# Kernel optimization log

Hardware: AMD Instinct MI355X
Metric: run time of the kernel (lower is better)

## Reference

```python
import jax, jax.numpy as jnp
import numpy as np

LEVEL = 3
NUM_BANDS = LEVEL + 1
B, N, D_MODEL, PATCH_NUMS, PRED_LEN = 32, 7, 768, 64, 336

# db4 lowpass decomposition filter (pywt convention)
_DB4_DEC_LO = np.array([
    -0.010597401784997278, 0.032883011666982945, 0.030841381835986965,
    -0.18703481171888114, -0.02798376941698385, 0.6308807679295904,
    0.7148465705525415, 0.23037781330885523], dtype=np.float32)
REC_LO = _DB4_DEC_LO[::-1].copy()                                   # reconstruction lowpass
REC_HI = (_DB4_DEC_LO * ((-1.0) ** (np.arange(8) + 1))).astype(np.float32)  # reconstruction highpass (QMF)


def _upsample2(x):
    # zero-interleave along last axis: (..., L) -> (..., 2L)
    z = jnp.zeros_like(x)
    return jnp.stack([x, z], axis=-1).reshape(*x.shape[:-1], 2 * x.shape[-1])


def _idwt_per(ca, cd, rec_lo, rec_hi):
    # single-level inverse DWT, periodization mode, along last axis: (..., L) -> (..., 2L)
    F = rec_lo.shape[0]
    ua, ud = _upsample2(ca), _upsample2(cd)
    y = jnp.zeros_like(ua)
    for k in range(F):  # small fixed tap loop (F=8)
        y = y + jnp.roll(ua, k, axis=-1) * rec_lo[k] + jnp.roll(ud, k, axis=-1) * rec_hi[k]
    return jnp.roll(y, -(F // 2 - 1), axis=-1)  # compensate filter delay


def _iswt(coeffs, level, rec_lo, rec_hi):
    # coeffs: (..., T, level+1) with bands ordered [cA, cD_level, ..., cD1]
    T = coeffs.shape[-2]
    out = coeffs[..., 0]
    for j in range(level, 0, -1):
        step = 2 ** (j - 1)
        cd = coeffs[..., level - j + 1]
        M = T // step
        # gather the `step` interleaved subsequences as a batch axis: (..., step, M)
        o = jnp.moveaxis(out.reshape(*out.shape[:-1], M, step), -1, -2)
        d = jnp.moveaxis(cd.reshape(*cd.shape[:-1], M, step), -1, -2)
        x1 = _idwt_per(o[..., 0::2], d[..., 0::2], rec_lo, rec_hi)
        x2 = jnp.roll(_idwt_per(o[..., 1::2], d[..., 1::2], rec_lo, rec_hi), 1, axis=-1)
        new = 0.5 * (x1 + x2)  # (..., step, M)
        out = jnp.moveaxis(new, -2, -1).reshape(*out.shape[:-1], T)
    return out


def setup_inputs() -> dict:
    key = jax.random.key(0)
    kx, kw, kb = jax.random.split(key, 3)
    Din = D_MODEL * PATCH_NUMS
    x = jax.random.normal(kx, (B, N, D_MODEL, PATCH_NUMS), dtype=jnp.float32)
    # Linear init ~ U(-1/sqrt(Din), 1/sqrt(Din)); small normal is equivalent for a reference
    W = jax.random.normal(kw, (NUM_BANDS, Din, PRED_LEN), dtype=jnp.float32) * (1.0 / np.sqrt(Din))
    b = jax.random.normal(kb, (NUM_BANDS, PRED_LEN), dtype=jnp.float32) * 0.01
    return {"x": x, "W": W, "b": b}


def reference(x, W, b):
    # x: (B, N, d_model, patch_nums); W: (bands, d_model*patch_nums, pred_len); b: (bands, pred_len)
    Bb, Nn, dm, P = x.shape
    xf = x.reshape(Bb, Nn, dm * P)  # Flatten(start_dim=-2)
    # all band projections as one batched GEMM -> (B, N, pred_len, bands)
    coeffs = jnp.einsum('bnd,kdp->bnpk', xf, W) + b.T
    rec_lo = jnp.asarray(REC_LO)
    rec_hi = jnp.asarray(REC_HI)
    return _iswt(coeffs, LEVEL, rec_lo, rec_hi)  # (B, N, pred_len)
```

## Files before the change

kernel.cpp:

```cpp
#include <hip/hip_runtime.h>
#include <stdint.h>

#define M_ROWS   224
#define K_DIM    49152
#define NCOL     1344
#define PRED     336
#define S_CHUNKS 24
#define STEPS    64


typedef __attribute__((ext_vector_type(8))) short short8;
typedef __attribute__((ext_vector_type(4))) float floatx4;

__device__ __forceinline__ uint16_t f32_to_bf16(float f) {
    uint32_t u = __builtin_bit_cast(uint32_t, f);
    uint32_t r = (u + 0x7fffu + ((u >> 16) & 1u)) >> 16;
    return (uint16_t)r;
}
__device__ __forceinline__ float bf16_to_f32(uint16_t h) {
    uint32_t u = ((uint32_t)h) << 16;
    return __builtin_bit_cast(float, u);
}
__device__ __forceinline__ uint32_t pack2(float lo, float hi) {
    return (uint32_t)f32_to_bf16(lo) | ((uint32_t)f32_to_bf16(hi) << 16);
}

__global__ __launch_bounds__(256, 2) void gemm_partial(
    const float* __restrict__ X,
    const float* __restrict__ W,
    uint16_t* __restrict__ P)
{
    __shared__ uint16_t lA[2][14 * 512];

    const int id = blockIdx.x;
    const int g  = id & 7;
    const int q  = id >> 3;
    const int ct = q % 21;
    const int s  = g + 8 * (q / 21);

    const int tid  = threadIdx.x;
    const int lane = tid & 63;
    const int w    = tid >> 6;
    const int l15  = lane & 15;
    const int kq   = lane >> 4;
    const int c0w  = ct * 64 + w * 16;
    const int band = c0w / PRED;
    const int p0   = c0w - band * PRED;

    const float* wbase = W + (size_t)band * ((size_t)K_DIM * PRED)
                           + (size_t)(kq * 8) * PRED
                           + (size_t)(p0 + l15);
    const float* xbase = X + (size_t)l15 * K_DIM + (size_t)(kq * 8);
    const int kbase = s * (STEPS * 32);

    floatx4 acc[14];
    #pragma unroll
    for (int f = 0; f < 14; ++f) acc[f] = (floatx4){0.f, 0.f, 0.f, 0.f};

    float wcur[8], wnxt[8];
    float4 xr[4][2];

    #pragma unroll
    for (int t = 0; t < 4; ++t) {
        const int f = w + 4 * t;
        if (f < 14) {
            const float* gp = xbase + (size_t)(16 * f) * K_DIM + kbase;
            xr[t][0] = *(const float4*)gp;
            xr[t][1] = *(const float4*)(gp + 4);
        }
    }
    #pragma unroll
    for (int j = 0; j < 8; ++j) wcur[j] = wbase[(size_t)(kbase + j) * PRED];
    #pragma unroll
    for (int t = 0; t < 4; ++t) {
        const int f = w + 4 * t;
        if (f < 14) {
            short8 v;
            ((uint32_t*)&v)[0] = pack2(xr[t][0].x, xr[t][0].y);
            ((uint32_t*)&v)[1] = pack2(xr[t][0].z, xr[t][0].w);
            ((uint32_t*)&v)[2] = pack2(xr[t][1].x, xr[t][1].y);
            ((uint32_t*)&v)[3] = pack2(xr[t][1].z, xr[t][1].w);
            *(short8*)&lA[0][f * 512 + lane * 8] = v;
        }
    }

    for (int st = 0; st < STEPS; ++st) {
        __syncthreads();
        const int cur = st & 1;

        if (st + 1 < STEPS) {
            const int kn = kbase + (st + 1) * 32;
            #pragma unroll
            for (int t = 0; t < 4; ++t) {
                const int f = w + 4 * t;
                if (f < 14) {
                    const float* gp = xbase + (size_t)(16 * f) * K_DIM + kn;
                    xr[t][0] = *(const float4*)gp;
                    xr[t][1] = *(const float4*)(gp + 4);
                }
            }
            #pragma unroll
            for (int j = 0; j < 8; ++j) wnxt[j] = wbase[(size_t)(kn + j) * PRED];
        }

        short8 bfrag;
        #pragma unroll
        for (int j = 0; j < 4; ++j)
            ((uint32_t*)&bfrag)[j] = pack2(wcur[2 * j], wcur[2 * j + 1]);

        #pragma unroll
        for (int f = 0; f < 14; ++f) {
            short8 afrag = *(const short8*)&lA[cur][f * 512 + lane * 8];
            acc[f] = __builtin_amdgcn_mfma_f32_16x16x32_bf16(afrag, bfrag, acc[f], 0, 0, 0);
        }

        if (st + 1 < STEPS) {
            #pragma unroll
            for (int t = 0; t < 4; ++t) {
                const int f = w + 4 * t;
                if (f < 14) {
                    short8 v;
                    ((uint32_t*)&v)[0] = pack2(xr[t][0].x, xr[t][0].y);
                    ((uint32_t*)&v)[1] = pack2(xr[t][0].z, xr[t][0].w);
                    ((uint32_t*)&v)[2] = pack2(xr[t][1].x, xr[t][1].y);
                    ((uint32_t*)&v)[3] = pack2(xr[t][1].z, xr[t][1].w);
                    *(short8*)&lA[cur ^ 1][f * 512 + lane * 8] = v;
                }
            }
            #pragma unroll
            for (int j = 0; j < 8; ++j) wcur[j] = wnxt[j];
        }
    }

    const int col = c0w + l15;
    #pragma unroll
    for (int f = 0; f < 14; ++f) {
        #pragma unroll
        for (int r = 0; r < 4; ++r) {
            const int m = 16 * f + kq * 4 + r;
            P[((size_t)m * S_CHUNKS + s) * NCOL + col] = f32_to_bf16(acc[f][r]);
        }
    }
}

__device__ const float REC_LO[8] = {
     0.23037781330885523f,  0.7148465705525415f,   0.6308807679295904f,
    -0.02798376941698385f, -0.18703481171888114f,  0.030841381835986965f,
     0.032883011666982945f, -0.010597401784997278f };
__device__ const float REC_HI[8] = {
     0.010597401784997278f, 0.032883011666982945f, -0.030841381835986965f,
    -0.18703481171888114f,  0.02798376941698385f,   0.6308807679295904f,
    -0.7148465705525415f,   0.23037781330885523f };

__global__ __launch_bounds__(1024) void reduce_iswt(
    const uint16_t* __restrict__ P,
    const float* __restrict__ bias,
    float* __restrict__ out)
{
    __shared__ float coeff[NCOL];
    __shared__ float buf[2][PRED];

    const int row = blockIdx.x;
    const int tid = threadIdx.x;
    const uint32_t* pr = (const uint32_t*)(P + (size_t)row * S_CHUNKS * NCOL);

    if (tid < NCOL / 2) {
        float a0 = 0.f, a1 = 0.f;
        #pragma unroll 8
        for (int s = 0; s < S_CHUNKS; ++s) {
            const uint32_t v = pr[s * (NCOL / 2) + tid];
            a0 += bf16_to_f32((uint16_t)(v & 0xffff));
            a1 += bf16_to_f32((uint16_t)(v >> 16));
        }
        coeff[2 * tid]     = a0 + bias[2 * tid];
        coeff[2 * tid + 1] = a1 + bias[2 * tid + 1];
    }
    __syncthreads();

    if (tid < PRED) buf[0][tid] = coeff[tid];
    __syncthreads();

    int curb = 0;
    for (int j = 3; j >= 1; --j) {
        const int step = 1 << (j - 1);
        const int M    = PRED / step;
        const float* cd  = &coeff[(4 - j) * PRED];
        const float* cur = buf[curb];
        float* nxt       = buf[curb ^ 1];
        if (tid < PRED) {
            const int t = tid;
            const int sidx = t & (step - 1);
            const int m = t / step;
            const int mm1 = (m == 0) ? (M - 1) : (m - 1);
            float x1 = 0.f, x2 = 0.f;
            #pragma unroll
            for (int k = 0; k < 8; ++k) {
                int i1 = m + 3 - k;  if (i1 < 0) i1 += M; else if (i1 >= M) i1 -= M;
                if ((i1 & 1) == 0) {
                    const int pos = i1 * step + sidx;
                    x1 += cur[pos] * REC_LO[k] + cd[pos] * REC_HI[k];
                }
                int i2 = mm1 + 3 - k;  if (i2 < 0) i2 += M; else if (i2 >= M) i2 -= M;
                if ((i2 & 1) == 0) {
                    const int pos = (i2 + 1) * step + sidx;
                    x2 += cur[pos] * REC_LO[k] + cd[pos] * REC_HI[k];
                }
            }
            nxt[t] = 0.5f * (x1 + x2);
        }
        __syncthreads();
        curb ^= 1;
    }

    if (tid < PRED) out[(size_t)row * PRED + tid] = buf[curb][tid];
}

extern "C" void kernel_launch(void* const* d_in, const int* in_sizes, int n_in,
                              void* d_out, int out_size, void* d_ws, size_t ws_size,
                              hipStream_t stream) {
    const float* X    = (const float*)d_in[0];
    const float* W    = (const float*)d_in[1];
    const float* bias = (const float*)d_in[2];
    float* out        = (float*)d_out;
    uint16_t* P       = (uint16_t*)d_ws;

    gemm_partial<<<21 * S_CHUNKS, 256, 0, stream>>>(X, W, P);
    reduce_iswt <<<M_ROWS, 1024, 0, stream>>>(P, bias, out);
}
```

Before: 518.0 us.

## Double split-K chunks, prefetch W two steps ahead, replace syncthreads with raw barrier

Doubles the number of K chunks, halving the steps per block, and raises the occupancy hint to 4 blocks per CU so more blocks fill the GPU. The main loop is unrolled by two with ping-pong W registers, so W loads are issued two steps ahead. __syncthreads is replaced by an explicit lgkmcnt wait plus s_barrier, which only waits on LDS traffic. The cost is twice as much bf16 partial output to write and reduce, plus tighter register pressure under the new launch bound.

```diff
diff --git a/kernel.cpp b/kernel.cpp
--- a/kernel.cpp
+++ b/kernel.cpp
@@ -5,8 +5,8 @@
 #define K_DIM    49152
 #define NCOL     1344
 #define PRED     336
-#define S_CHUNKS 24
-#define STEPS    64
+#define S_CHUNKS 48
+#define STEPS    32
 
 
 typedef __attribute__((ext_vector_type(8))) short short8;
@@ -22,10 +22,11 @@
     return __builtin_bit_cast(float, u);
 }
 __device__ __forceinline__ uint32_t pack2(float lo, float hi) {
-    return (uint32_t)f32_to_bf16(lo) | ((uint32_t)f32_to_bf16(hi) << 16);
-}
-
-__global__ __launch_bounds__(256, 2) void gemm_partial(
+    uint32_t r = (uint32_t)f32_to_bf16(lo) | ((uint32_t)f32_to_bf16(hi) << 16);
+    return r;
+}
+
+__global__ __launch_bounds__(256, 4) void gemm_partial(
     const float* __restrict__ X,
     const float* __restrict__ W,
     uint16_t* __restrict__ P)
@@ -57,7 +58,7 @@
     #pragma unroll
     for (int f = 0; f < 14; ++f) acc[f] = (floatx4){0.f, 0.f, 0.f, 0.f};
 
-    float wcur[8], wnxt[8];
+    float wA[8], wB[8];
     float4 xr[4][2];
 
     #pragma unroll
@@ -70,7 +71,9 @@
         }
     }
     #pragma unroll
-    for (int j = 0; j < 8; ++j) wcur[j] = wbase[(size_t)(kbase + j) * PRED];
+    for (int j = 0; j < 8; ++j) wA[j] = wbase[(size_t)(kbase + j) * PRED];
+    #pragma unroll
+    for (int j = 0; j < 8; ++j) wB[j] = wbase[(size_t)(kbase + 32 + j) * PRED];
     #pragma unroll
     for (int t = 0; t < 4; ++t) {
         const int f = w + 4 * t;
@@ -83,54 +86,62 @@
             *(short8*)&lA[0][f * 512 + lane * 8] = v;
         }
     }
-
-    for (int st = 0; st < STEPS; ++st) {
-        __syncthreads();
-        const int cur = st & 1;
-
-        if (st + 1 < STEPS) {
-            const int kn = kbase + (st + 1) * 32;
-            #pragma unroll
-            for (int t = 0; t < 4; ++t) {
-                const int f = w + 4 * t;
-                if (f < 14) {
-                    const float* gp = xbase + (size_t)(16 * f) * K_DIM + kn;
-                    xr[t][0] = *(const float4*)gp;
-                    xr[t][1] = *(const float4*)(gp + 4);
-                }
-            }
-            #pragma unroll
-            for (int j = 0; j < 8; ++j) wnxt[j] = wbase[(size_t)(kn + j) * PRED];
-        }
-
-        short8 bfrag;
-        #pragma unroll
-        for (int j = 0; j < 4; ++j)
-            ((uint32_t*)&bfrag)[j] = pack2(wcur[2 * j], wcur[2 * j + 1]);
-
-        #pragma unroll
-        for (int f = 0; f < 14; ++f) {
-            short8 afrag = *(const short8*)&lA[cur][f * 512 + lane * 8];
-            acc[f] = __builtin_amdgcn_mfma_f32_16x16x32_bf16(afrag, bfrag, acc[f], 0, 0, 0);
-        }
-
-        if (st + 1 < STEPS) {
-            #pragma unroll
-            for (int t = 0; t < 4; ++t) {
-                const int f = w + 4 * t;
-                if (f < 14) {
-                    short8 v;
-                    ((uint32_t*)&v)[0] = pack2(xr[t][0].x, xr[t][0].y);
-                    ((uint32_t*)&v)[1] = pack2(xr[t][0].z, xr[t][0].w);
-                    ((uint32_t*)&v)[2] = pack2(xr[t][1].x, xr[t][1].y);
-                    ((uint32_t*)&v)[3] = pack2(xr[t][1].z, xr[t][1].w);
-                    *(short8*)&lA[cur ^ 1][f * 512 + lane * 8] = v;
-                }
-            }
-            #pragma unroll
-            for (int j = 0; j < 8; ++j) wcur[j] = wnxt[j];
-        }
-    }
+    asm volatile("s_waitcnt lgkmcnt(0)" ::: "memory");
+    __builtin_amdgcn_s_barrier();
+
+#define GEMM_STEP(WREG, RBUF, WBUF, ST)                                        \
+    {                                                                          \
+        short8 bfrag;                                                          \
+        _Pragma("unroll")                                                      \
+        for (int j = 0; j < 4; ++j)                                            \
+            ((uint32_t*)&bfrag)[j] = pack2(WREG[2*j], WREG[2*j+1]);            \
+        if ((ST) + 1 < STEPS) {                                                \
+            const int kx = kbase + ((ST) + 1) * 32;                            \
+            _Pragma("unroll")                                                  \
+            for (int t = 0; t < 4; ++t) {                                      \
+                const int f = w + 4 * t;                                       \
+                if (f < 14) {                                                  \
+                    const float* gp = xbase + (size_t)(16 * f) * K_DIM + kx;   \
+                    xr[t][0] = *(const float4*)gp;                             \
+                    xr[t][1] = *(const float4*)(gp + 4);                       \
+                }                                                              \
+            }                                                                  \
+        }                                                                      \
+        if ((ST) + 2 < STEPS) {                                                \
+            const int kw2 = kbase + ((ST) + 2) * 32;                           \
+            _Pragma("unroll")                                                  \
+            for (int j = 0; j < 8; ++j)                                        \
+                WREG[j] = wbase[(size_t)(kw2 + j) * PRED];                     \
+        }                                                                      \
+        _Pragma("unroll")                                                      \
+        for (int f = 0; f < 14; ++f) {                                         \
+            short8 afrag = *(const short8*)&lA[RBUF][f * 512 + lane * 8];      \
+            acc[f] = __builtin_amdgcn_mfma_f32_16x16x32_bf16(                  \
+                afrag, bfrag, acc[f], 0, 0, 0);                                \
+        }                                                                      \
+        if ((ST) + 1 < STEPS) {                                                \
+            _Pragma("unroll")                                                  \
+            for (int t = 0; t < 4; ++t) {                                      \
+                const int f = w + 4 * t;                                       \
+                if (f < 14) {                                                  \
+                    short8 v;                                                  \
+                    ((uint32_t*)&v)[0] = pack2(xr[t][0].x, xr[t][0].y);        \
+                    ((uint32_t*)&v)[1] = pack2(xr[t][0].z, xr[t][0].w);        \
+                    ((uint32_t*)&v)[2] = pack2(xr[t][1].x, xr[t][1].y);        \
+                    ((uint32_t*)&v)[3] = pack2(xr[t][1].z, xr[t][1].w);        \
+                    *(short8*)&lA[WBUF][f * 512 + lane * 8] = v;               \
+                }                                                              \
+            }                                                                  \
+        }                                                                      \
+        asm volatile("s_waitcnt lgkmcnt(0)" ::: "memory");                     \
+        __builtin_amdgcn_s_barrier();                                          \
+    }
+
+    for (int st = 0; st < STEPS; st += 2) {
+        GEMM_STEP(wA, 0, 1, st)
+        GEMM_STEP(wB, 1, 0, st + 1)
+    }
+#undef GEMM_STEP
 
     const int col = c0w + l15;
     #pragma unroll
```

After: 632.2 us. +22.0%, slower.
